# Kernel tuning notes

Measured on AMD Instinct MI355X. Metric: run time of the kernel, lower is better.

## Reference

```python
import jax, jax.numpy as jnp
import numpy as np

B, V, CIN, COUT, TDIM = 2, 65536, 128, 256, 512
EPS = 1e-5
G1, G2 = 32, 32  # _gn_num_groups(128)=32, _gn_num_groups(256)=32


def group_norm(x, w, b, groups):
    # x: [B, V, C]; torch GroupNorm on [B, C, V] normalizes per (batch, group)
    # over the group's channels AND all V positions (biased variance).
    Bx, Vx, C = x.shape
    xr = x.reshape(Bx, Vx, groups, C // groups)
    mean = xr.mean(axis=(1, 3), keepdims=True)
    var = xr.var(axis=(1, 3), keepdims=True)
    xn = ((xr - mean) * jax.lax.rsqrt(var + EPS)).reshape(Bx, Vx, C)
    return xn * w + b


def neigh_conv(x, neigh, W, b):
    # x: [B, V, C]; neigh: [V, 9]; W: [out, 9*C]; b: [out]
    C = x.shape[-1]
    gathered = x[:, neigh]                      # [B, V, 9, C]
    Wr = W.reshape(-1, 9, C)                    # [out, 9, C]
    return jnp.einsum('bvnc,onc->bvo', gathered, Wr) + b


def setup_inputs() -> dict:
    key = jax.random.key(0)
    ks = jax.random.split(key, 12)
    s = 0.02
    return {
        'x': jax.random.normal(ks[0], (B, V, CIN), jnp.float32),
        't_emb': jax.random.normal(ks[1], (B, TDIM), jnp.float32),
        'neigh_orders': jax.random.randint(ks[2], (V, 9), 0, V, jnp.int64)
            if jax.config.jax_enable_x64 else jax.random.randint(ks[2], (V, 9), 0, V, jnp.int32),
        'gn1_w': jnp.ones((CIN,), jnp.float32),
        'gn1_b': jnp.zeros((CIN,), jnp.float32),
        'w1': jax.random.normal(ks[3], (COUT, 9 * CIN), jnp.float32) * s,
        'b1': jnp.zeros((COUT,), jnp.float32),
        'wt': jax.random.normal(ks[4], (COUT, TDIM), jnp.float32) * s,
        'bt': jnp.zeros((COUT,), jnp.float32),
        'gn2_w': jnp.ones((COUT,), jnp.float32),
        'gn2_b': jnp.zeros((COUT,), jnp.float32),
        'w2': jax.random.normal(ks[5], (COUT, 9 * COUT), jnp.float32) * s,
        'b2': jnp.zeros((COUT,), jnp.float32),
        'ws': jax.random.normal(ks[6], (COUT, CIN), jnp.float32) * s,
        'bs': jnp.zeros((COUT,), jnp.float32),
    }


def reference(x, t_emb, neigh_orders, gn1_w, gn1_b, w1, b1, wt, bt,
              gn2_w, gn2_b, w2, b2, ws, bs):
    h = group_norm(x, gn1_w, gn1_b, G1)
    h = jax.nn.silu(h)
    h = neigh_conv(h, neigh_orders, w1, b1)                 # [B, V, COUT]
    t = jax.nn.silu(t_emb) @ wt.T + bt                      # [B, COUT]
    h = h + t[:, None, :]
    h = group_norm(h, gn2_w, gn2_b, G2)
    h = jax.nn.silu(h)
    h = neigh_conv(h, neigh_orders, w2, b2)                 # [B, V, COUT]
    shortcut = x @ ws.T + bs                                # learned 1x1 (in_ch != out_ch)
    return h + shortcut
```

## Files before the change

### kernel.cpp

```cpp
#include <hip/hip_runtime.h>
#include <hip/hip_bf16.h>

#define DEV __device__ __forceinline__

typedef __attribute__((ext_vector_type(8))) short bf16x8;
typedef __attribute__((ext_vector_type(4))) float f32x4;

constexpr int Bb = 2, V = 65536, CIN = 128, COUT = 256, TDIM = 512;
constexpr float EPS = 1e-5f;
constexpr int K1 = 1152, K2 = 2304, K2e = 2432;
constexpr int NCH1 = 128;
constexpr int NCH2 = 256;
constexpr int W1N = (K1/8)*COUT*8;
constexpr int W2N = (K2e/8)*COUT*8;

DEV float silu_f(float x){ return x / (1.f + __expf(-x)); }
DEV unsigned short f2b(float x){
  union { float f; unsigned u; } v; v.f = x;
  unsigned r = v.u + 0x7fffu + ((v.u >> 16) & 1u);
  return (unsigned short)(r >> 16);
}
DEV float b2f(unsigned short h){ union { unsigned u; float f; } v; v.u = ((unsigned)h) << 16; return v.f; }

__global__ void k_gn1_partial(const float* __restrict__ x, float* __restrict__ part){
  int b = blockIdx.y, ch = blockIdx.x;
  int t = threadIdx.x;
  int g  = t & 31;
  int r0 = t >> 5;
  float s = 0.f, ss = 0.f;
  const float4* xp = (const float4*)(x + ((size_t)b*V + (size_t)ch*512)*CIN) + g;
  for (int r = r0; r < 512; r += 8){
    float4 v = xp[(size_t)r*32];
    s  += v.x + v.y + v.z + v.w;
    ss += v.x*v.x + v.y*v.y + v.z*v.z + v.w*v.w;
  }
  __shared__ float s_s[8][32], s_q[8][32];
  s_s[r0][g] = s; s_q[r0][g] = ss; __syncthreads();
  if (t < 32){
    float a = 0, q = 0;
    #pragma unroll
    for (int i = 0; i < 8; ++i){ a += s_s[i][t]; q += s_q[i][t]; }
    int idx = ((b*32 + t)*NCH1 + ch)*2;
    part[idx] = a; part[idx+1] = q;
  }
}

__global__ void k_gn1_final(const float* __restrict__ part, const float* __restrict__ w,
                            const float* __restrict__ bias, float* __restrict__ sc,
                            float* __restrict__ bi){
  int t = threadIdx.x;
  if (t >= Bb*32) return;
  float s = 0, q = 0;
  for (int ch = 0; ch < NCH1; ++ch){ s += part[(t*NCH1+ch)*2]; q += part[(t*NCH1+ch)*2+1]; }
  float n = (float)V * 4.f;
  float mean = s / n;
  float var = q / n - mean*mean;
  float inv = rsqrtf(var + EPS);
  int b = t >> 5, g = t & 31;
  for (int j = 0; j < 4; ++j){
    int c = g*4 + j;
    float scl = w[c] * inv;
    sc[b*CIN + c] = scl;
    bi[b*CIN + c] = bias[c] - mean*scl;
  }
}

__global__ void k_act1(const float* __restrict__ x, const float* __restrict__ sc,
                       const float* __restrict__ bi, unsigned short* __restrict__ act1,
                       unsigned short* __restrict__ xb){
  size_t i = ((size_t)blockIdx.x*256 + threadIdx.x)*4;
  int c = (int)(i & (CIN-1));
  int b = (int)(i >> 23);
  float4 v = *(const float4*)(x + i);
  const float* scp = sc + b*CIN + c;
  const float* bip = bi + b*CIN + c;
  ushort4 a, xo;
  a.x = f2b(silu_f(v.x*scp[0] + bip[0]));
  a.y = f2b(silu_f(v.y*scp[1] + bip[1]));
  a.z = f2b(silu_f(v.z*scp[2] + bip[2]));
  a.w = f2b(silu_f(v.w*scp[3] + bip[3]));
  xo.x = f2b(v.x); xo.y = f2b(v.y); xo.z = f2b(v.z); xo.w = f2b(v.w);
  *(ushort4*)(act1 + i) = a;
  *(ushort4*)(xb + i)   = xo;
}

__global__ void k_prepW(const float* __restrict__ w1, const float* __restrict__ w2,
                        const float* __restrict__ wsm, unsigned short* __restrict__ W1b,
                        unsigned short* __restrict__ W2b){
  int i = blockIdx.x*256 + threadIdx.x;
  if (i < W1N){
    int j = i & 7, o = (i >> 3) & 255, k8 = i >> 11;
    W1b[i] = f2b(w1[o*K1 + k8*8 + j]);
  }
  int i2 = i - W1N;
  if (i2 >= 0 && i2 < W2N){
    int j = i2 & 7, o = (i2 >> 3) & 255, k8 = i2 >> 11;
    int k = k8*8 + j;
    float v = (k < K2) ? w2[o*K2 + k] : wsm[o*CIN + (k - K2)];
    W2b[i2] = f2b(v);
  }
}

__global__ void k_tcomb(const float* __restrict__ temb, const float* __restrict__ wt,
                        const float* __restrict__ bt, const float* __restrict__ b1,
                        float* __restrict__ tc){
  int b = blockIdx.y;
  int o = blockIdx.x*4 + (threadIdx.x >> 6);
  int l = threadIdx.x & 63;
  const float* tb = temb + (size_t)b*TDIM;
  const float* wr = wt + (size_t)o*TDIM;
  float acc = 0.f;
  #pragma unroll
  for (int k = l; k < TDIM; k += 64)
    acc += silu_f(tb[k]) * wr[k];
  #pragma unroll
  for (int off = 32; off > 0; off >>= 1) acc += __shfl_down(acc, off, 64);
  if (l == 0) tc[b*COUT + o] = acc + bt[o] + b1[o];
}

template<int CINR, int NCHUNK, int CPN, bool CONV2>
__launch_bounds__(512, 4)
__global__ void k_conv(const unsigned short* __restrict__ act,
                       const unsigned short* __restrict__ xb,
                       const unsigned short* __restrict__ Wb,
                       const int* __restrict__ neigh,
                       const float* __restrict__ tc,
                       const float* __restrict__ b2,
                       const float* __restrict__ bs,
                       unsigned short* __restrict__ outb,
                       float* __restrict__ outf){
  __shared__ __align__(16) unsigned short A_lds[2][128*64];
  __shared__ int nb[128*9];
  const int tid = threadIdx.x;
  const int w = tid >> 6, lane = tid & 63;
  const int bx = blockIdx.x;
  const int vflat = bx << 7;
  const int b = vflat >> 16;
  const int vb = vflat & (V-1);
  for (int i = tid; i < 128*9; i += 512) nb[i] = neigh[(size_t)vb*9 + i];

  f32x4 acc[4][4] = {};
  const int wm = w >> 2, wn = w & 3;
  const int quad = lane >> 4, l15 = lane & 15;
  const int sr = lane >> 3, ssg = lane & 7;

  const unsigned short* actb = act + (size_t)b*V*CINR;
  const unsigned short* xbb  = CONV2 ? (xb + (size_t)b*V*CIN) : (const unsigned short*)nullptr;
  const unsigned short* wq = Wb + (size_t)quad*COUT*8 + (size_t)((wn<<6) + l15)*8;

  auto STAGE_A = [&](int chunk, int buf){
    const bool scseg = CONV2 && (chunk >= NCHUNK-2);
    int nidx = 0, c0, rl;
    const unsigned short* src;
    if (scseg){ c0 = (chunk - (NCHUNK-2))*64; src = xbb; rl = CIN; }
    else      { nidx = chunk / CPN; c0 = (chunk % CPN)*64; src = actb; rl = CINR; }
    #pragma unroll
    for (int i = 0; i < 2; ++i){
      int row  = (w<<4) + (i<<3) + sr;
      int rowg = scseg ? (vb + row) : nb[row*9 + nidx];
      int g = ssg ^ (row & 7);
      const unsigned short* gp = src + (size_t)rowg*rl + c0 + g*8;
      unsigned short* lp = &A_lds[buf][((w<<4) + (i<<3))<<6];
      __builtin_amdgcn_global_load_lds(gp, lp, 16, 0, 0);
    }
  };

  auto LOADB = [&](int chunk, bf16x8 (&bv)[8]){
    const unsigned short* wp = wq + (size_t)chunk*8*COUT*8;
    #pragma unroll
    for (int nt = 0; nt < 4; ++nt){
      bv[nt*2+0] = *(const bf16x8*)(wp + (nt<<7));
      bv[nt*2+1] = *(const bf16x8*)(wp + 4*COUT*8 + (nt<<7));
    }
  };

  auto COMPUTE = [&](int cur, bf16x8 (&bv)[8]){
    __builtin_amdgcn_s_setprio(1);
    #pragma unroll
    for (int ks = 0; ks < 2; ++ks){
      bf16x8 av[4];
      #pragma unroll
      for (int mt = 0; mt < 4; ++mt){
        int m = (wm<<6) + (mt<<4) + l15;
        int seg = ((ks<<2) + quad) ^ (l15 & 7);
        av[mt] = *(const bf16x8*)&A_lds[cur][(m<<6) + (seg<<3)];
      }
      #pragma unroll
      for (int mt = 0; mt < 4; ++mt)
        #pragma unroll
        for (int nt = 0; nt < 4; ++nt)
          acc[mt][nt] = __builtin_amdgcn_mfma_f32_16x16x32_bf16(av[mt], bv[nt*2+ks], acc[mt][nt], 0, 0, 0);
    }
    __builtin_amdgcn_s_setprio(0);
  };

  __syncthreads();
  STAGE_A(0, 0);

  #pragma unroll 1
  for (int t = 0; t < NCHUNK-1; ++t){
    const int cur = t & 1;
    bf16x8 bv[8];
    LOADB(t, bv);
    STAGE_A(t+1, cur^1);
    asm volatile("s_waitcnt vmcnt(10)" ::: "memory");
    __builtin_amdgcn_s_barrier();
    asm volatile("" ::: "memory");
    COMPUTE(cur, bv);
    asm volatile("" ::: "memory");
    __builtin_amdgcn_s_barrier();
    asm volatile("" ::: "memory");
  }
  {
    bf16x8 bv[8];
    LOADB(NCHUNK-1, bv);
    asm volatile("s_waitcnt vmcnt(8)" ::: "memory");
    __builtin_amdgcn_s_barrier();
    asm volatile("" ::: "memory");
    COMPUTE((NCHUNK-1) & 1, bv);
  }

  #pragma unroll
  for (int mt = 0; mt < 4; ++mt){
    #pragma unroll
    for (int nt = 0; nt < 4; ++nt){
      int col = (wn<<6) + (nt<<4) + l15;
      float bval = CONV2 ? (b2[col] + bs[col]) : tc[b*COUT + col];
      #pragma unroll
      for (int rg = 0; rg < 4; ++rg){
        int row = (wm<<6) + (mt<<4) + (quad<<2) + rg;
        size_t off = ((size_t)(vflat + row))*COUT + col;
        float v = acc[mt][nt][rg] + bval;
        if (CONV2) outf[off] = v;
        else       outb[off] = f2b(v);
      }
    }
  }
}

__global__ void k_gn2_partial(const unsigned short* __restrict__ h1, float* __restrict__ part){
  int b = blockIdx.y, ch = blockIdx.x;
  int t = threadIdx.x;
  int g  = t & 31;
  int r0 = t >> 5;
  float s = 0.f, ss = 0.f;
  const unsigned short* p = h1 + ((size_t)b*V + (size_t)ch*256)*COUT + g*8;
  for (int r = r0; r < 256; r += 8){
    bf16x8 hv = *(const bf16x8*)(p + (size_t)r*COUT);
    #pragma unroll
    for (int j = 0; j < 8; ++j){
      float v = b2f((unsigned short)hv[j]);
      s += v; ss += v*v;
    }
  }
  __shared__ float s_s[8][32], s_q[8][32];
  s_s[r0][g] = s; s_q[r0][g] = ss; __syncthreads();
  if (t < 32){
    float a = 0, q = 0;
    #pragma unroll
    for (int i = 0; i < 8; ++i){ a += s_s[i][t]; q += s_q[i][t]; }
    int idx = ((b*32 + t)*NCH2 + ch)*2;
    part[idx] = a; part[idx+1] = q;
  }
}

__global__ void k_gn2_final(const float* __restrict__ part, const float* __restrict__ w,
                            const float* __restrict__ bias, float* __restrict__ sc,
                            float* __restrict__ bi){
  int t = threadIdx.x;
  if (t >= Bb*32) return;
  float s = 0, q = 0;
  for (int ch = 0; ch < NCH2; ++ch){ s += part[(t*NCH2+ch)*2]; q += part[(t*NCH2+ch)*2+1]; }
  float n = (float)V * 8.f;
  float mean = s / n, var = q / n - mean*mean, inv = rsqrtf(var + EPS);
  int b = t >> 5, g = t & 31;
  for (int j = 0; j < 8; ++j){
    int c = g*8 + j;
    float scl = w[c] * inv;
    sc[b*COUT + c] = scl;
    bi[b*COUT + c] = bias[c] - mean*scl;
  }
}

__global__ void k_act2(unsigned short* __restrict__ h1, const float* __restrict__ sc,
                       const float* __restrict__ bi){
  size_t i = ((size_t)blockIdx.x*256 + threadIdx.x)*8;
  int c = (int)(i & (COUT-1));
  int b = (int)(i >> 24);
  bf16x8 h = *(const bf16x8*)(h1 + i);
  const float* scp = sc + b*COUT + c;
  const float* bip = bi + b*COUT + c;
  bf16x8 o;
  #pragma unroll
  for (int j = 0; j < 8; ++j)
    o[j] = (short)f2b(silu_f(b2f((unsigned short)h[j])*scp[j] + bip[j]));
  *(bf16x8*)(h1 + i) = o;
}

extern "C" void kernel_launch(void* const* d_in, const int* in_sizes, int n_in,
                              void* d_out, int out_size, void* d_ws, size_t ws_size,
                              hipStream_t stream){
  const float* x    = (const float*)d_in[0];
  const float* temb = (const float*)d_in[1];
  const int*   neigh= (const int*)d_in[2];
  const float* gn1w = (const float*)d_in[3];
  const float* gn1b = (const float*)d_in[4];
  const float* w1   = (const float*)d_in[5];
  const float* b1   = (const float*)d_in[6];
  const float* wt   = (const float*)d_in[7];
  const float* bt   = (const float*)d_in[8];
  const float* gn2w = (const float*)d_in[9];
  const float* gn2b = (const float*)d_in[10];
  const float* w2   = (const float*)d_in[11];
  const float* b2   = (const float*)d_in[12];
  const float* wsm  = (const float*)d_in[13];
  const float* bs   = (const float*)d_in[14];
  float* out = (float*)d_out;

  char* wsp = (char*)d_ws;
  unsigned short* act1 = (unsigned short*)(wsp);
  unsigned short* xb   = (unsigned short*)(wsp + 33554432);
  unsigned short* h1   = (unsigned short*)(wsp + 67108864);
  unsigned short* W1b  = (unsigned short*)(wsp + 134217728);
  unsigned short* W2b  = (unsigned short*)(wsp + 134217728 + 589824);
  char* p = wsp + 134217728 + 589824 + 1245184;
  float* tc    = (float*)p;  p += 2048;
  float* part1 = (float*)p;  p += (size_t)Bb*32*NCH1*2*4;
  float* part2 = (float*)p;  p += (size_t)Bb*32*NCH2*2*4;
  float* sc1   = (float*)p;  p += 1024;
  float* bi1   = (float*)p;  p += 1024;
  float* sc2   = (float*)p;  p += 2048;
  float* bi2   = (float*)p;  p += 2048;

  k_gn1_partial<<<dim3(NCH1, Bb), 256, 0, stream>>>(x, part1);
  k_gn1_final  <<<1, 64, 0, stream>>>(part1, gn1w, gn1b, sc1, bi1);
  k_act1       <<<16384, 256, 0, stream>>>(x, sc1, bi1, act1, xb);
  k_prepW      <<<(W1N + W2N)/256, 256, 0, stream>>>(w1, w2, wsm, W1b, W2b);
  k_tcomb      <<<dim3(COUT/4, Bb), 256, 0, stream>>>(temb, wt, bt, b1, tc);
  k_conv<128, 18, 2, false><<<1024, 512, 0, stream>>>(act1, nullptr, W1b, neigh, tc, nullptr, nullptr, h1, nullptr);
  k_gn2_partial<<<dim3(NCH2, Bb), 256, 0, stream>>>(h1, part2);
  k_gn2_final  <<<1, 64, 0, stream>>>(part2, gn2w, gn2b, sc2, bi2);
  k_act2       <<<16384, 256, 0, stream>>>(h1, sc2, bi2);
  k_conv<256, 38, 4, true><<<1024, 512, 0, stream>>>(h1, xb, W2b, neigh, nullptr, b2, bs, nullptr, out);
}
```

Before: 542.4 us.

## Split conv K-chunk into two halves with interleaved loads and MFMAs

Restructures the conv GEMM main loop so each K chunk is processed in two halves. Each half issues its own LDS reads of A and global loads of B right before its 16 MFMAs, and the prefetch of the next A tile is placed between them. The final vmcnt(0) wait moves to the end of the iteration, and the peeled last iteration is folded into the loop with guards. The aim is to overlap global-to-LDS staging with compute and to cut register pressure from holding all eight B fragments. The trade-off is a full vmcnt(0) drain each iteration and extra barriers.

```diff
diff --git a/kernel.cpp b/kernel.cpp
--- a/kernel.cpp
+++ b/kernel.cpp
@@ -165,59 +165,60 @@
     }
   };
 
-  auto LOADB = [&](int chunk, bf16x8 (&bv)[8]){
-    const unsigned short* wp = wq + (size_t)chunk*8*COUT*8;
-    #pragma unroll
-    for (int nt = 0; nt < 4; ++nt){
-      bv[nt*2+0] = *(const bf16x8*)(wp + (nt<<7));
-      bv[nt*2+1] = *(const bf16x8*)(wp + 4*COUT*8 + (nt<<7));
+  auto LOADB_H = [&](int chunk, int half, bf16x8 (&bv)[4]){
+    const unsigned short* wp = wq + (size_t)chunk*8*COUT*8 + (half ? 4*COUT*8 : 0);
+    #pragma unroll
+    for (int nt = 0; nt < 4; ++nt) bv[nt] = *(const bf16x8*)(wp + (nt<<7));
+  };
+
+  auto DSREAD_A = [&](int cur, int ks, bf16x8 (&av)[4]){
+    #pragma unroll
+    for (int mt = 0; mt < 4; ++mt){
+      int m = (wm<<6) + (mt<<4) + l15;
+      int seg = ((ks<<2) + quad) ^ (l15 & 7);
+      av[mt] = *(const bf16x8*)&A_lds[cur][(m<<6) + (seg<<3)];
     }
   };
 
-  auto COMPUTE = [&](int cur, bf16x8 (&bv)[8]){
+  auto MFMA16 = [&](bf16x8 (&av)[4], bf16x8 (&bv)[4]){
     __builtin_amdgcn_s_setprio(1);
     #pragma unroll
-    for (int ks = 0; ks < 2; ++ks){
-      bf16x8 av[4];
+    for (int mt = 0; mt < 4; ++mt)
       #pragma unroll
-      for (int mt = 0; mt < 4; ++mt){
-        int m = (wm<<6) + (mt<<4) + l15;
-        int seg = ((ks<<2) + quad) ^ (l15 & 7);
-        av[mt] = *(const bf16x8*)&A_lds[cur][(m<<6) + (seg<<3)];
-      }
-      #pragma unroll
-      for (int mt = 0; mt < 4; ++mt)
-        #pragma unroll
-        for (int nt = 0; nt < 4; ++nt)
-          acc[mt][nt] = __builtin_amdgcn_mfma_f32_16x16x32_bf16(av[mt], bv[nt*2+ks], acc[mt][nt], 0, 0, 0);
-    }
+      for (int nt = 0; nt < 4; ++nt)
+        acc[mt][nt] = __builtin_amdgcn_mfma_f32_16x16x32_bf16(av[mt], bv[nt], acc[mt][nt], 0, 0, 0);
     __builtin_amdgcn_s_setprio(0);
   };
 
   __syncthreads();
   STAGE_A(0, 0);
+  asm volatile("s_waitcnt vmcnt(0)" ::: "memory");
+  __builtin_amdgcn_s_barrier();
+  asm volatile("" ::: "memory");
 
   #pragma unroll 1
-  for (int t = 0; t < NCHUNK-1; ++t){
+  for (int t = 0; t < NCHUNK; ++t){
     const int cur = t & 1;
-    bf16x8 bv[8];
-    LOADB(t, bv);
-    STAGE_A(t+1, cur^1);
-    asm volatile("s_waitcnt vmcnt(10)" ::: "memory");
+    bf16x8 av0[4], bv0[4];
+    DSREAD_A(cur, 0, av0);
+    LOADB_H(t, 0, bv0);
+    if (t+1 < NCHUNK) STAGE_A(t+1, cur^1);
+    asm volatile("" ::: "memory");
     __builtin_amdgcn_s_barrier();
     asm volatile("" ::: "memory");
-    COMPUTE(cur, bv);
+    MFMA16(av0, bv0);
     asm volatile("" ::: "memory");
     __builtin_amdgcn_s_barrier();
     asm volatile("" ::: "memory");
-  }
-  {
-    bf16x8 bv[8];
-    LOADB(NCHUNK-1, bv);
-    asm volatile("s_waitcnt vmcnt(8)" ::: "memory");
+    bf16x8 av1[4], bv1[4];
+    LOADB_H(t, 1, bv1);
+    DSREAD_A(cur, 1, av1);
+    MFMA16(av1, bv1);
+    if (t+1 < NCHUNK)
+      asm volatile("s_waitcnt vmcnt(0)" ::: "memory");
+    asm volatile("" ::: "memory");
     __builtin_amdgcn_s_barrier();
     asm volatile("" ::: "memory");
-    COMPUTE((NCHUNK-1) & 1, bv);
   }
 
   #pragma unroll
```

After: 560.3 us. 3.3% more time.
